# Performance work log

Measured on AMD Instinct MI355X. Metric: run time of the kernel, lower is better.

Reference implementation:

```python
import jax, jax.numpy as jnp
import numpy as np

BLOCK = 32      # block_size
KB = 128        # K // BLOCK (mask rows)
NB = 128        # N // BLOCK (mask cols)
DENSITY = 0.1


def _make_mask_indices():
    rng = np.random.RandomState(0)
    mask = rng.rand(KB, NB) < DENSITY
    # guarantee no fully-empty output column (kernel writes zeros there anyway,
    # segment_sum also yields zeros, so this is only to keep stats sane)
    ii, jj = np.nonzero(mask)   # row-major order == torch.nonzero(mask)
    return ii.astype(np.int32), jj.astype(np.int32)


def setup_inputs() -> dict:
    key = jax.random.key(0)
    k1, k2 = jax.random.split(key)
    ii, jj = _make_mask_indices()
    nnz = ii.shape[0]
    M = 4096
    K = KB * BLOCK
    x = jax.random.normal(k1, (M, K), dtype=jnp.float32)
    # block-sparse weight: one [BLOCK, BLOCK] tile per nonzero mask entry,
    # stored in row-major nonzero order (matches torch.nonzero ordering)
    w = jax.random.normal(k2, (nnz, BLOCK, BLOCK), dtype=jnp.float32) * 0.02
    return {"x": x, "w": w, "idx_i": jnp.asarray(ii), "idx_j": jnp.asarray(jj)}


def reference(x, w, idx_i, idx_j):
    # y[:, j*B:(j+1)*B] += x[:, i*B:(i+1)*B] @ w[blk] for each nonzero block (i, j)
    M, K = x.shape
    nnz, B, _ = w.shape
    xb = x.reshape(M, K // B, B)[:, idx_i, :]                 # [M, nnz, B] gather
    partial = jnp.einsum('mnk,nkj->nmj', xb, w)               # [nnz, M, B]
    yb = jax.ops.segment_sum(partial, idx_j, num_segments=NB)  # [NB, M, B] scatter-add
    return yb.transpose(1, 0, 2).reshape(M, NB * B)           # [M, N]
```

## Files before the change

kernel.cpp:

```cpp
#include <hip/hip_runtime.h>
#include <hip/hip_bf16.h>

typedef __bf16 bf16x8 __attribute__((ext_vector_type(8)));
typedef __bf16 bf16x4 __attribute__((ext_vector_type(4)));
typedef float f32x4 __attribute__((ext_vector_type(4)));

#define KDIM 4096
#define NDIM 4096
#define NBJ  128
#define KB   128

__global__ __launch_bounds__(256) void k_prep(
    const float* __restrict__ x, const float* __restrict__ w,
    const int* __restrict__ idx_i, const int* __restrict__ idx_j,
    __bf16* __restrict__ xb, __bf16* __restrict__ wT,
    int* __restrict__ colptr, int* __restrict__ colinfo,
    int nnz, int M, int nbCvt) {
    __shared__ char smem[2176];
    int b = blockIdx.x, t = threadIdx.x;

    if (b < nbCvt) {
        int i  = b & (KB - 1);
        int m0 = (b >> 7) * 64;
        int q  = t & 3, r = t >> 2;
        const float* xp = x + (size_t)(m0 + r) * KDIM + i * 32 + q * 8;
        float4 u = ((const float4*)xp)[0];
        float4 v = ((const float4*)xp)[1];
        bf16x8 o;
        o[0]=(__bf16)u.x; o[1]=(__bf16)u.y; o[2]=(__bf16)u.z; o[3]=(__bf16)u.w;
        o[4]=(__bf16)v.x; o[5]=(__bf16)v.y; o[6]=(__bf16)v.z; o[7]=(__bf16)v.w;
        *(bf16x8*)(xb + ((size_t)i * M + m0 + r) * 32 + q * 8) = o;
    } else if (b < nbCvt + nnz) {
        auto tile = (__bf16(*)[33])smem;
        int n = b - nbCvt;
        float4 v = ((const float4*)(w + (size_t)n * 1024))[t];
        int e = t * 4, k = e >> 5, c = e & 31;
        tile[k][c + 0] = (__bf16)v.x; tile[k][c + 1] = (__bf16)v.y;
        tile[k][c + 2] = (__bf16)v.z; tile[k][c + 3] = (__bf16)v.w;
        __syncthreads();
        int f = t * 4, cc = f >> 5, kk = f & 31;
        bf16x4 o;
        o[0] = tile[kk + 0][cc]; o[1] = tile[kk + 1][cc];
        o[2] = tile[kk + 2][cc]; o[3] = tile[kk + 3][cc];
        ((bf16x4*)(wT + (size_t)n * 1024))[t] = o;
    } else {
        int* cnt = (int*)smem;
        int* cur = cnt + NBJ;
        if (t < NBJ) cnt[t] = 0;
        __syncthreads();
        for (int n = t; n < nnz; n += 256) atomicAdd(&cnt[idx_j[n]], 1);
        __syncthreads();
        int mycount = (t < NBJ) ? cnt[t] : 0;
        for (int off = 1; off < NBJ; off <<= 1) {
            int add = (t < NBJ && t >= off) ? cnt[t - off] : 0;
            __syncthreads();
            if (t < NBJ) cnt[t] += add;
            __syncthreads();
        }
        if (t < NBJ) {
            colptr[t + 1] = cnt[t];
            cur[t] = cnt[t] - mycount;
            if (t == 0) colptr[0] = 0;
        }
        __syncthreads();
        for (int n = t; n < nnz; n += 256) {
            int j = idx_j[n];
            int pos = atomicAdd(&cur[j], 1);
            colinfo[pos] = (idx_i[n] << 16) | n;
        }
    }
}

struct Frag { bf16x8 a0, a1, a2, a3, b0, b1; };

__global__ __launch_bounds__(256) void k_bsmm(
    const __bf16* __restrict__ xb, const __bf16* __restrict__ wT,
    const int* __restrict__ colptr, const int* __restrict__ colinfo,
    float* __restrict__ y, int M) {
    int RCH = M >> 8;
    int l = blockIdx.x;
    int rc, j;
    if ((RCH & 7) == 0) {
        int rps = RCH >> 3;
        int s = l & 7, u = l >> 3;
        rc = s * rps + (u % rps);
        j  = u / rps;
    } else {
        rc = l % RCH; j = l / RCH;
    }
    int lane = threadIdx.x & 63, wave = threadIdx.x >> 6;
    int quad = lane >> 4, l16 = lane & 15;
    int wrow = rc * 256 + wave * 64;

    int beg = colptr[j], end = colptr[j + 1];
    int cnt = end - beg;

    f32x4 acc[4][2] = {};

    if (cnt > 0) {
        size_t strideA = (size_t)M * 32;
        const __bf16* xbase = xb + (size_t)(wrow + l16) * 32 + quad * 8;
        const __bf16* wbase = wT + l16 * 32 + quad * 8;
        int cap = cnt - 1;

        if (cnt <= 64) {
            int einfo = colinfo[beg + (lane <= cap ? lane : cap)];
            auto fetch = [&](int p) {
                int pp = p <= cap ? p : cap;
                int ee = __shfl(einfo, pp);
                int n = ee & 0xFFFF, ib = ee >> 16;
                Frag f;
                const __bf16* xp = xbase + (size_t)ib * strideA;
                f.a0 = *(const bf16x8*)(xp);
                f.a1 = *(const bf16x8*)(xp + 16 * 32);
                f.a2 = *(const bf16x8*)(xp + 32 * 32);
                f.a3 = *(const bf16x8*)(xp + 48 * 32);
                const __bf16* wp = wbase + (size_t)n * 1024;
                f.b0 = *(const bf16x8*)(wp);
                f.b1 = *(const bf16x8*)(wp + 512);
                return f;
            };
            Frag f0 = fetch(0);
            Frag f1 = fetch(1);
            for (int p = 0; p < cnt; ++p) {
                acc[0][0] = __builtin_amdgcn_mfma_f32_16x16x32_bf16(f0.a0, f0.b0, acc[0][0], 0, 0, 0);
                acc[0][1] = __builtin_amdgcn_mfma_f32_16x16x32_bf16(f0.a0, f0.b1, acc[0][1], 0, 0, 0);
                acc[1][0] = __builtin_amdgcn_mfma_f32_16x16x32_bf16(f0.a1, f0.b0, acc[1][0], 0, 0, 0);
                acc[1][1] = __builtin_amdgcn_mfma_f32_16x16x32_bf16(f0.a1, f0.b1, acc[1][1], 0, 0, 0);
                acc[2][0] = __builtin_amdgcn_mfma_f32_16x16x32_bf16(f0.a2, f0.b0, acc[2][0], 0, 0, 0);
                acc[2][1] = __builtin_amdgcn_mfma_f32_16x16x32_bf16(f0.a2, f0.b1, acc[2][1], 0, 0, 0);
                acc[3][0] = __builtin_amdgcn_mfma_f32_16x16x32_bf16(f0.a3, f0.b0, acc[3][0], 0, 0, 0);
                acc[3][1] = __builtin_amdgcn_mfma_f32_16x16x32_bf16(f0.a3, f0.b1, acc[3][1], 0, 0, 0);
                f0 = f1;
                f1 = fetch(p + 2);
            }
        } else {
            auto fetch = [&](int p) {
                int pp = p <= cap ? p : cap;
                int ee = colinfo[beg + pp];
                int n = ee & 0xFFFF, ib = ee >> 16;
                Frag f;
                const __bf16* xp = xbase + (size_t)ib * strideA;
                f.a0 = *(const bf16x8*)(xp);
                f.a1 = *(const bf16x8*)(xp + 16 * 32);
                f.a2 = *(const bf16x8*)(xp + 32 * 32);
                f.a3 = *(const bf16x8*)(xp + 48 * 32);
                const __bf16* wp = wbase + (size_t)n * 1024;
                f.b0 = *(const bf16x8*)(wp);
                f.b1 = *(const bf16x8*)(wp + 512);
                return f;
            };
            Frag f0 = fetch(0);
            Frag f1 = fetch(1);
            for (int p = 0; p < cnt; ++p) {
                acc[0][0] = __builtin_amdgcn_mfma_f32_16x16x32_bf16(f0.a0, f0.b0, acc[0][0], 0, 0, 0);
                acc[0][1] = __builtin_amdgcn_mfma_f32_16x16x32_bf16(f0.a0, f0.b1, acc[0][1], 0, 0, 0);
                acc[1][0] = __builtin_amdgcn_mfma_f32_16x16x32_bf16(f0.a1, f0.b0, acc[1][0], 0, 0, 0);
                acc[1][1] = __builtin_amdgcn_mfma_f32_16x16x32_bf16(f0.a1, f0.b1, acc[1][1], 0, 0, 0);
                acc[2][0] = __builtin_amdgcn_mfma_f32_16x16x32_bf16(f0.a2, f0.b0, acc[2][0], 0, 0, 0);
                acc[2][1] = __builtin_amdgcn_mfma_f32_16x16x32_bf16(f0.a2, f0.b1, acc[2][1], 0, 0, 0);
                acc[3][0] = __builtin_amdgcn_mfma_f32_16x16x32_bf16(f0.a3, f0.b0, acc[3][0], 0, 0, 0);
                acc[3][1] = __builtin_amdgcn_mfma_f32_16x16x32_bf16(f0.a3, f0.b1, acc[3][1], 0, 0, 0);
                f0 = f1;
                f1 = fetch(p + 2);
            }
        }
    }

    #pragma unroll
    for (int r = 0; r < 4; ++r)
        #pragma unroll
        for (int ch = 0; ch < 2; ++ch)
            #pragma unroll
            for (int reg = 0; reg < 4; ++reg) {
                int row = wrow + r * 16 + quad * 4 + reg;
                int col = j * 32 + ch * 16 + l16;
                y[(size_t)row * NDIM + col] = acc[r][ch][reg];
            }
}

__global__ __launch_bounds__(256) void k_bsmm_nows(
    const float* __restrict__ x, const float* __restrict__ w,
    const int* __restrict__ idx_i, const int* __restrict__ idx_j,
    float* __restrict__ y, int nnz) {
    __shared__ int list[256];
    __shared__ int listn;
    __shared__ __bf16 tw[32][40];
    int j = blockIdx.y;
    int tid = threadIdx.x;
    int lane = tid & 63, wave = tid >> 6;
    int quad = lane >> 4, l16 = lane & 15;
    int wrow = blockIdx.x * 256 + wave * 64;

    if (tid == 0) listn = 0;
    __syncthreads();
    for (int n = tid; n < nnz; n += 256)
        if (idx_j[n] == j) { int p = atomicAdd(&listn, 1); list[p & 255] = n; }
    __syncthreads();
    int cnt = listn;

    f32x4 acc[4][2] = {};
    for (int p = 0; p < cnt; ++p) {
        int n = list[p];
        int ib = idx_i[n];
        {
            float4 v = ((const float4*)(w + (size_t)n * 1024))[tid];
            int e = tid * 4, k = e >> 5, c = e & 31;
            tw[c + 0][k] = (__bf16)v.x; tw[c + 1][k] = (__bf16)v.y;
            tw[c + 2][k] = (__bf16)v.z; tw[c + 3][k] = (__bf16)v.w;
        }
        __syncthreads();
        bf16x8 a[4];
        #pragma unroll
        for (int r = 0; r < 4; ++r) {
            const float* xp = x + (size_t)(wrow + r * 16 + l16) * KDIM + ib * 32 + quad * 8;
            float4 u = *(const float4*)(xp);
            float4 v = *(const float4*)(xp + 4);
            a[r][0] = (__bf16)u.x; a[r][1] = (__bf16)u.y; a[r][2] = (__bf16)u.z; a[r][3] = (__bf16)u.w;
            a[r][4] = (__bf16)v.x; a[r][5] = (__bf16)v.y; a[r][6] = (__bf16)v.z; a[r][7] = (__bf16)v.w;
        }
        bf16x8 b0 = *(const bf16x8*)&tw[l16][quad * 8];
        bf16x8 b1 = *(const bf16x8*)&tw[l16 + 16][quad * 8];
        #pragma unroll
        for (int r = 0; r < 4; ++r) {
            acc[r][0] = __builtin_amdgcn_mfma_f32_16x16x32_bf16(a[r], b0, acc[r][0], 0, 0, 0);
            acc[r][1] = __builtin_amdgcn_mfma_f32_16x16x32_bf16(a[r], b1, acc[r][1], 0, 0, 0);
        }
        __syncthreads();
    }

    #pragma unroll
    for (int r = 0; r < 4; ++r)
        #pragma unroll
        for (int ch = 0; ch < 2; ++ch)
            #pragma unroll
            for (int reg = 0; reg < 4; ++reg) {
                int row = wrow + r * 16 + quad * 4 + reg;
                int col = j * 32 + ch * 16 + l16;
                y[(size_t)row * NDIM + col] = acc[r][ch][reg];
            }
}

extern "C" void kernel_launch(void* const* d_in, const int* in_sizes, int n_in,
                              void* d_out, int out_size, void* d_ws, size_t ws_size,
                              hipStream_t stream) {
    const float* x     = (const float*)d_in[0];
    const float* w     = (const float*)d_in[1];
    const int*   idx_i = (const int*)d_in[2];
    const int*   idx_j = (const int*)d_in[3];
    float*       y     = (float*)d_out;

    int nnz = in_sizes[2];
    int M   = in_sizes[0] / KDIM;

    size_t xb_bytes = (size_t)M * KDIM * 2;
    size_t wt_bytes = (size_t)nnz * 1024 * 2;
    size_t need = xb_bytes + wt_bytes + (size_t)(NBJ + 2 + nnz) * 4;

    if (ws_size >= need && (M & 255) == 0) {
        __bf16* xb      = (__bf16*)d_ws;
        __bf16* wT      = (__bf16*)((char*)d_ws + xb_bytes);
        int*    colptr  = (int*)((char*)d_ws + xb_bytes + wt_bytes);
        int*    colinfo = colptr + NBJ + 1;
        int nbCvt = KB * (M / 64);
        k_prep<<<nbCvt + nnz + 1, 256, 0, stream>>>(x, w, idx_i, idx_j,
                                                    xb, wT, colptr, colinfo,
                                                    nnz, M, nbCvt);
        k_bsmm<<<(M / 256) * NBJ, 256, 0, stream>>>(xb, wT, colptr, colinfo, y, M);
    } else {
        k_bsmm_nows<<<dim3(M / 256, NBJ), 256, 0, stream>>>(x, w, idx_i, idx_j, y, nnz);
    }
}
```

Baseline: 172.4 us.

## Fuse prep and block-sparse matmul into one cooperative kernel with grid sync

Replaces the separate conversion/CSR-build kernel and the MFMA matmul kernel with a single cooperative kernel. Each block first converts its slice of x to bf16, some blocks transpose weight tiles, and the last block builds column pointers, then a grid-wide sync precedes the matmul tile. This removes a kernel launch boundary and the tail/launch gap between them, at the cost of a grid barrier and requiring all 2048 blocks to be co-resident (launch bounds raised to 8 blocks per CU), which may increase register pressure. Falls back to the two-kernel path if the cooperative launch fails.

```diff
diff --git a/kernel.cpp b/kernel.cpp
--- a/kernel.cpp
+++ b/kernel.cpp
@@ -1,5 +1,8 @@
 #include <hip/hip_runtime.h>
+#include <hip/hip_cooperative_groups.h>
 #include <hip/hip_bf16.h>
+
+namespace cg = cooperative_groups;
 
 typedef __bf16 bf16x8 __attribute__((ext_vector_type(8)));
 typedef __bf16 bf16x4 __attribute__((ext_vector_type(4)));
@@ -9,6 +12,183 @@
 #define NDIM 4096
 #define NBJ  128
 #define KB   128
+
+__device__ __forceinline__ void bsmm_tile(
+    const __bf16* __restrict__ xb, const __bf16* __restrict__ wT,
+    const int* __restrict__ colptr, const int* __restrict__ colinfo,
+    float* __restrict__ y, int M, int rc, int j) {
+    int lane = threadIdx.x & 63, wave = threadIdx.x >> 6;
+    int quad = lane >> 4, l16 = lane & 15;
+    int wrow = rc * 256 + wave * 64;
+
+    int beg = colptr[j], end = colptr[j + 1];
+    int cnt = end - beg;
+
+    f32x4 acc[4][2] = {};
+
+    if (cnt > 0) {
+        size_t strideA = (size_t)M * 32;
+        const __bf16* xbase = xb + (size_t)(wrow + l16) * 32 + quad * 8;
+        const __bf16* wbase = wT + l16 * 32 + quad * 8;
+        int cap = cnt - 1;
+
+        if (cnt <= 64) {
+            int einfo = colinfo[beg + (lane <= cap ? lane : cap)];
+            auto fetch = [&](int p) {
+                int pp = p <= cap ? p : cap;
+                int ee = __shfl(einfo, pp);
+                int n = ee & 0xFFFF, ib = ee >> 16;
+                struct { bf16x8 a0, a1, a2, a3, b0, b1; } f;
+                const __bf16* xp = xbase + (size_t)ib * strideA;
+                f.a0 = *(const bf16x8*)(xp);
+                f.a1 = *(const bf16x8*)(xp + 16 * 32);
+                f.a2 = *(const bf16x8*)(xp + 32 * 32);
+                f.a3 = *(const bf16x8*)(xp + 48 * 32);
+                const __bf16* wp = wbase + (size_t)n * 1024;
+                f.b0 = *(const bf16x8*)(wp);
+                f.b1 = *(const bf16x8*)(wp + 512);
+                return f;
+            };
+            auto f0 = fetch(0);
+            auto f1 = fetch(1);
+            for (int p = 0; p < cnt; ++p) {
+                acc[0][0] = __builtin_amdgcn_mfma_f32_16x16x32_bf16(f0.a0, f0.b0, acc[0][0], 0, 0, 0);
+                acc[0][1] = __builtin_amdgcn_mfma_f32_16x16x32_bf16(f0.a0, f0.b1, acc[0][1], 0, 0, 0);
+                acc[1][0] = __builtin_amdgcn_mfma_f32_16x16x32_bf16(f0.a1, f0.b0, acc[1][0], 0, 0, 0);
+                acc[1][1] = __builtin_amdgcn_mfma_f32_16x16x32_bf16(f0.a1, f0.b1, acc[1][1], 0, 0, 0);
+                acc[2][0] = __builtin_amdgcn_mfma_f32_16x16x32_bf16(f0.a2, f0.b0, acc[2][0], 0, 0, 0);
+                acc[2][1] = __builtin_amdgcn_mfma_f32_16x16x32_bf16(f0.a2, f0.b1, acc[2][1], 0, 0, 0);
+                acc[3][0] = __builtin_amdgcn_mfma_f32_16x16x32_bf16(f0.a3, f0.b0, acc[3][0], 0, 0, 0);
+                acc[3][1] = __builtin_amdgcn_mfma_f32_16x16x32_bf16(f0.a3, f0.b1, acc[3][1], 0, 0, 0);
+                f0 = f1;
+                f1 = fetch(p + 2);
+            }
+        } else {
+            auto fetch = [&](int p) {
+                int pp = p <= cap ? p : cap;
+                int ee = colinfo[beg + pp];
+                int n = ee & 0xFFFF, ib = ee >> 16;
+                struct { bf16x8 a0, a1, a2, a3, b0, b1; } f;
+                const __bf16* xp = xbase + (size_t)ib * strideA;
+                f.a0 = *(const bf16x8*)(xp);
+                f.a1 = *(const bf16x8*)(xp + 16 * 32);
+                f.a2 = *(const bf16x8*)(xp + 32 * 32);
+                f.a3 = *(const bf16x8*)(xp + 48 * 32);
+                const __bf16* wp = wbase + (size_t)n * 1024;
+                f.b0 = *(const bf16x8*)(wp);
+                f.b1 = *(const bf16x8*)(wp + 512);
+                return f;
+            };
+            auto f0 = fetch(0);
+            auto f1 = fetch(1);
+            for (int p = 0; p < cnt; ++p) {
+                acc[0][0] = __builtin_amdgcn_mfma_f32_16x16x32_bf16(f0.a0, f0.b0, acc[0][0], 0, 0, 0);
+                acc[0][1] = __builtin_amdgcn_mfma_f32_16x16x32_bf16(f0.a0, f0.b1, acc[0][1], 0, 0, 0);
+                acc[1][0] = __builtin_amdgcn_mfma_f32_16x16x32_bf16(f0.a1, f0.b0, acc[1][0], 0, 0, 0);
+                acc[1][1] = __builtin_amdgcn_mfma_f32_16x16x32_bf16(f0.a1, f0.b1, acc[1][1], 0, 0, 0);
+                acc[2][0] = __builtin_amdgcn_mfma_f32_16x16x32_bf16(f0.a2, f0.b0, acc[2][0], 0, 0, 0);
+                acc[2][1] = __builtin_amdgcn_mfma_f32_16x16x32_bf16(f0.a2, f0.b1, acc[2][1], 0, 0, 0);
+                acc[3][0] = __builtin_amdgcn_mfma_f32_16x16x32_bf16(f0.a3, f0.b0, acc[3][0], 0, 0, 0);
+                acc[3][1] = __builtin_amdgcn_mfma_f32_16x16x32_bf16(f0.a3, f0.b1, acc[3][1], 0, 0, 0);
+                f0 = f1;
+                f1 = fetch(p + 2);
+            }
+        }
+    }
+
+    #pragma unroll
+    for (int r = 0; r < 4; ++r)
+        #pragma unroll
+        for (int ch = 0; ch < 2; ++ch)
+            #pragma unroll
+            for (int reg = 0; reg < 4; ++reg) {
+                int row = wrow + r * 16 + quad * 4 + reg;
+                int col = j * 32 + ch * 16 + l16;
+                y[(size_t)row * NDIM + col] = acc[r][ch][reg];
+            }
+}
+
+__global__ __launch_bounds__(256, 8) void k_fused(
+    const float* __restrict__ x, const float* __restrict__ w,
+    const int* __restrict__ idx_i, const int* __restrict__ idx_j,
+    __bf16* __restrict__ xb, __bf16* __restrict__ wT,
+    int* __restrict__ colptr, int* __restrict__ colinfo,
+    float* __restrict__ y, int nnz, int M) {
+    __shared__ char smem[2176];
+    int l = blockIdx.x, t = threadIdx.x;
+    int RCH = M >> 8;
+
+    int rc, j;
+    if ((RCH & 7) == 0) {
+        int rps = RCH >> 3;
+        int s = l & 7, u = l >> 3;
+        rc = s * rps + (u % rps);
+        j  = u / rps;
+    } else {
+        rc = l % RCH; j = l / RCH;
+    }
+
+    {
+        int q = t & 3, r = t >> 2;
+        #pragma unroll
+        for (int it = 0; it < 4; ++it) {
+            int row = rc * 256 + it * 64 + r;
+            const float* xp = x + (size_t)row * KDIM + j * 32 + q * 8;
+            float4 u4 = ((const float4*)xp)[0];
+            float4 v4 = ((const float4*)xp)[1];
+            bf16x8 o;
+            o[0]=(__bf16)u4.x; o[1]=(__bf16)u4.y; o[2]=(__bf16)u4.z; o[3]=(__bf16)u4.w;
+            o[4]=(__bf16)v4.x; o[5]=(__bf16)v4.y; o[6]=(__bf16)v4.z; o[7]=(__bf16)v4.w;
+            *(bf16x8*)(xb + ((size_t)j * M + row) * 32 + q * 8) = o;
+        }
+    }
+
+    for (int n = l; n < nnz; n += gridDim.x) {
+        auto tile = (__bf16(*)[33])smem;
+        float4 v = ((const float4*)(w + (size_t)n * 1024))[t];
+        int e = t * 4, k = e >> 5, c = e & 31;
+        tile[k][c + 0] = (__bf16)v.x; tile[k][c + 1] = (__bf16)v.y;
+        tile[k][c + 2] = (__bf16)v.z; tile[k][c + 3] = (__bf16)v.w;
+        __syncthreads();
+        int f = t * 4, cc = f >> 5, kk = f & 31;
+        bf16x4 o;
+        o[0] = tile[kk + 0][cc]; o[1] = tile[kk + 1][cc];
+        o[2] = tile[kk + 2][cc]; o[3] = tile[kk + 3][cc];
+        ((bf16x4*)(wT + (size_t)n * 1024))[t] = o;
+        __syncthreads();
+    }
+
+    if (l == gridDim.x - 1) {
+        int* cnt = (int*)smem;
+        int* cur = cnt + NBJ;
+        if (t < NBJ) cnt[t] = 0;
+        __syncthreads();
+        for (int n = t; n < nnz; n += 256) atomicAdd(&cnt[idx_j[n]], 1);
+        __syncthreads();
+        int mycount = (t < NBJ) ? cnt[t] : 0;
+        for (int off = 1; off < NBJ; off <<= 1) {
+            int add = (t < NBJ && t >= off) ? cnt[t - off] : 0;
+            __syncthreads();
+            if (t < NBJ) cnt[t] += add;
+            __syncthreads();
+        }
+        if (t < NBJ) {
+            colptr[t + 1] = cnt[t];
+            cur[t] = cnt[t] - mycount;
+            if (t == 0) colptr[0] = 0;
+        }
+        __syncthreads();
+        for (int n = t; n < nnz; n += 256) {
+            int jj = idx_j[n];
+            int pos = atomicAdd(&cur[jj], 1);
+            colinfo[pos] = (idx_i[n] << 16) | n;
+        }
+    }
+
+    cg::this_grid().sync();
+
+    bsmm_tile(xb, wT, colptr, colinfo, y, M, rc, j);
+}
 
 __global__ __launch_bounds__(256) void k_prep(
     const float* __restrict__ x, const float* __restrict__ w,
@@ -64,14 +244,12 @@
         }
         __syncthreads();
         for (int n = t; n < nnz; n += 256) {
-            int j = idx_j[n];
-            int pos = atomicAdd(&cur[j], 1);
+            int jj = idx_j[n];
+            int pos = atomicAdd(&cur[jj], 1);
             colinfo[pos] = (idx_i[n] << 16) | n;
         }
     }
 }
-
-struct Frag { bf16x8 a0, a1, a2, a3, b0, b1; };
 
 __global__ __launch_bounds__(256) void k_bsmm(
     const __bf16* __restrict__ xb, const __bf16* __restrict__ wT,
@@ -88,95 +266,7 @@
     } else {
         rc = l % RCH; j = l / RCH;
     }
-    int lane = threadIdx.x & 63, wave = threadIdx.x >> 6;
-    int quad = lane >> 4, l16 = lane & 15;
-    int wrow = rc * 256 + wave * 64;
-
-    int beg = colptr[j], end = colptr[j + 1];
-    int cnt = end - beg;
-
-    f32x4 acc[4][2] = {};
-
-    if (cnt > 0) {
-        size_t strideA = (size_t)M * 32;
-        const __bf16* xbase = xb + (size_t)(wrow + l16) * 32 + quad * 8;
-        const __bf16* wbase = wT + l16 * 32 + quad * 8;
-        int cap = cnt - 1;
-
-        if (cnt <= 64) {
-            int einfo = colinfo[beg + (lane <= cap ? lane : cap)];
-            auto fetch = [&](int p) {
-                int pp = p <= cap ? p : cap;
-                int ee = __shfl(einfo, pp);
-                int n = ee & 0xFFFF, ib = ee >> 16;
-                Frag f;
-                const __bf16* xp = xbase + (size_t)ib * strideA;
-                f.a0 = *(const bf16x8*)(xp);
-                f.a1 = *(const bf16x8*)(xp + 16 * 32);
-                f.a2 = *(const bf16x8*)(xp + 32 * 32);
-                f.a3 = *(const bf16x8*)(xp + 48 * 32);
-                const __bf16* wp = wbase + (size_t)n * 1024;
-                f.b0 = *(const bf16x8*)(wp);
-                f.b1 = *(const bf16x8*)(wp + 512);
-                return f;
-            };
-            Frag f0 = fetch(0);
-            Frag f1 = fetch(1);
-            for (int p = 0; p < cnt; ++p) {
-                acc[0][0] = __builtin_amdgcn_mfma_f32_16x16x32_bf16(f0.a0, f0.b0, acc[0][0], 0, 0, 0);
-                acc[0][1] = __builtin_amdgcn_mfma_f32_16x16x32_bf16(f0.a0, f0.b1, acc[0][1], 0, 0, 0);
-                acc[1][0] = __builtin_amdgcn_mfma_f32_16x16x32_bf16(f0.a1, f0.b0, acc[1][0], 0, 0, 0);
-                acc[1][1] = __builtin_amdgcn_mfma_f32_16x16x32_bf16(f0.a1, f0.b1, acc[1][1], 0, 0, 0);
-                acc[2][0] = __builtin_amdgcn_mfma_f32_16x16x32_bf16(f0.a2, f0.b0, acc[2][0], 0, 0, 0);
-                acc[2][1] = __builtin_amdgcn_mfma_f32_16x16x32_bf16(f0.a2, f0.b1, acc[2][1], 0, 0, 0);
-                acc[3][0] = __builtin_amdgcn_mfma_f32_16x16x32_bf16(f0.a3, f0.b0, acc[3][0], 0, 0, 0);
-                acc[3][1] = __builtin_amdgcn_mfma_f32_16x16x32_bf16(f0.a3, f0.b1, acc[3][1], 0, 0, 0);
-                f0 = f1;
-                f1 = fetch(p + 2);
-            }
-        } else {
-            auto fetch = [&](int p) {
-                int pp = p <= cap ? p : cap;
-                int ee = colinfo[beg + pp];
-                int n = ee & 0xFFFF, ib = ee >> 16;
-                Frag f;
-                const __bf16* xp = xbase + (size_t)ib * strideA;
-                f.a0 = *(const bf16x8*)(xp);
-                f.a1 = *(const bf16x8*)(xp + 16 * 32);
-                f.a2 = *(const bf16x8*)(xp + 32 * 32);
-                f.a3 = *(const bf16x8*)(xp + 48 * 32);
-                const __bf16* wp = wbase + (size_t)n * 1024;
-                f.b0 = *(const bf16x8*)(wp);
-                f.b1 = *(const bf16x8*)(wp + 512);
-                return f;
-            };
-            Frag f0 = fetch(0);
-            Frag f1 = fetch(1);
-            for (int p = 0; p < cnt; ++p) {
-                acc[0][0] = __builtin_amdgcn_mfma_f32_16x16x32_bf16(f0.a0, f0.b0, acc[0][0], 0, 0, 0);
-                acc[0][1] = __builtin_amdgcn_mfma_f32_16x16x32_bf16(f0.a0, f0.b1, acc[0][1], 0, 0, 0);
-                acc[1][0] = __builtin_amdgcn_mfma_f32_16x16x32_bf16(f0.a1, f0.b0, acc[1][0], 0, 0, 0);
-                acc[1][1] = __builtin_amdgcn_mfma_f32_16x16x32_bf16(f0.a1, f0.b1, acc[1][1], 0, 0, 0);
-                acc[2][0] = __builtin_amdgcn_mfma_f32_16x16x32_bf16(f0.a2, f0.b0, acc[2][0], 0, 0, 0);
-                acc[2][1] = __builtin_amdgcn_mfma_f32_16x16x32_bf16(f0.a2, f0.b1, acc[2][1], 0, 0, 0);
-                acc[3][0] = __builtin_amdgcn_mfma_f32_16x16x32_bf16(f0.a3, f0.b0, acc[3][0], 0, 0, 0);
-                acc[3][1] = __builtin_amdgcn_mfma_f32_16x16x32_bf16(f0.a3, f0.b1, acc[3][1], 0, 0, 0);
-                f0 = f1;
-                f1 = fetch(p + 2);
-            }
-        }
-    }
-
-    #pragma unroll
-    for (int r = 0; r < 4; ++r)
-        #pragma unroll
-        for (int ch = 0; ch < 2; ++ch)
-            #pragma unroll
-            for (int reg = 0; reg < 4; ++reg) {
-                int row = wrow + r * 16 + quad * 4 + reg;
-                int col = j * 32 + ch * 16 + l16;
-                y[(size_t)row * NDIM + col] = acc[r][ch][reg];
-            }
+    bsmm_tile(xb, wT, colptr, colinfo, y, M, rc, j);
 }
 
 __global__ __launch_bounds__(256) void k_bsmm_nows(
@@ -262,11 +352,21 @@
         __bf16* wT      = (__bf16*)((char*)d_ws + xb_bytes);
         int*    colptr  = (int*)((char*)d_ws + xb_bytes + wt_bytes);
         int*    colinfo = colptr + NBJ + 1;
-        int nbCvt = KB * (M / 64);
-        k_prep<<<nbCvt + nnz + 1, 256, 0, stream>>>(x, w, idx_i, idx_j,
-                                                    xb, wT, colptr, colinfo,
-                                                    nnz, M, nbCvt);
-        k_bsmm<<<(M / 256) * NBJ, 256, 0, stream>>>(xb, wT, colptr, colinfo, y, M);
+
+        int grid = (M / 256) * NBJ;
+        void* args[] = {(void*)&x, (void*)&w, (void*)&idx_i, (void*)&idx_j,
+                        (void*)&xb, (void*)&wT, (void*)&colptr, (void*)&colinfo,
+                        (void*)&y, (void*)&nnz, (void*)&M};
+        hipError_t err = hipLaunchCooperativeKernel(
+            (const void*)k_fused, dim3(grid), dim3(256), args, 0, stream);
+        if (err != hipSuccess) {
+            (void)hipGetLastError();
+            int nbCvt = KB * (M / 64);
+            k_prep<<<nbCvt + nnz + 1, 256, 0, stream>>>(x, w, idx_i, idx_j,
+                                                        xb, wT, colptr, colinfo,
+                                                        nnz, M, nbCvt);
+            k_bsmm<<<(M / 256) * NBJ, 256, 0, stream>>>(xb, wT, colptr, colinfo, y, M);
+        }
     } else {
         k_bsmm_nows<<<dim3(M / 256, NBJ), 256, 0, stream>>>(x, w, idx_i, idx_j, y, nnz);
     }
```

Result: slower. 429.9 us (+149.4%).

## Stage weight blocks in padded LDS per column and deepen A-fragment prefetch

Applied to the files above, without the earlier changes.

The bsmm kernel now loads batches of up to 14 weight tiles for its output column into shared memory, padded to avoid bank conflicts, and has all four waves read B fragments from LDS. Previously each wave fetched them from global memory. The A-fragment prefetch grows from two to three stages, the block-index mapping becomes j-major using shifts and masks, and launch bounds request 4 blocks per CU. This should cut redundant global weight traffic and hide x-load latency better, at the cost of extra barriers per batch and about 35 KB of LDS per block, which may limit occupancy.

```diff
diff --git a/kernel.cpp b/kernel.cpp
--- a/kernel.cpp
+++ b/kernel.cpp
@@ -9,6 +9,9 @@
 #define NDIM 4096
 #define NBJ  128
 #define KB   128
+
+#define NB      14
+#define BLK_LDS 2560
 
 __global__ __launch_bounds__(256) void k_prep(
     const float* __restrict__ x, const float* __restrict__ w,
@@ -71,99 +74,83 @@
     }
 }
 
-struct Frag { bf16x8 a0, a1, a2, a3, b0, b1; };
-
-__global__ __launch_bounds__(256) void k_bsmm(
+struct AFrag { bf16x8 a0, a1, a2, a3; };
+
+#define MFMA8(A, B0, B1)                                                       \
+    acc[0][0] = __builtin_amdgcn_mfma_f32_16x16x32_bf16(A.a0, B0, acc[0][0], 0, 0, 0); \
+    acc[0][1] = __builtin_amdgcn_mfma_f32_16x16x32_bf16(A.a0, B1, acc[0][1], 0, 0, 0); \
+    acc[1][0] = __builtin_amdgcn_mfma_f32_16x16x32_bf16(A.a1, B0, acc[1][0], 0, 0, 0); \
+    acc[1][1] = __builtin_amdgcn_mfma_f32_16x16x32_bf16(A.a1, B1, acc[1][1], 0, 0, 0); \
+    acc[2][0] = __builtin_amdgcn_mfma_f32_16x16x32_bf16(A.a2, B0, acc[2][0], 0, 0, 0); \
+    acc[2][1] = __builtin_amdgcn_mfma_f32_16x16x32_bf16(A.a2, B1, acc[2][1], 0, 0, 0); \
+    acc[3][0] = __builtin_amdgcn_mfma_f32_16x16x32_bf16(A.a3, B0, acc[3][0], 0, 0, 0); \
+    acc[3][1] = __builtin_amdgcn_mfma_f32_16x16x32_bf16(A.a3, B1, acc[3][1], 0, 0, 0);
+
+__global__ __launch_bounds__(256, 4) void k_bsmm(
     const __bf16* __restrict__ xb, const __bf16* __restrict__ wT,
     const int* __restrict__ colptr, const int* __restrict__ colinfo,
     float* __restrict__ y, int M) {
+    __shared__ int nfo[NB];
+    __shared__ __attribute__((aligned(16))) char wbuf[NB * BLK_LDS];
+
     int RCH = M >> 8;
     int l = blockIdx.x;
     int rc, j;
     if ((RCH & 7) == 0) {
         int rps = RCH >> 3;
         int s = l & 7, u = l >> 3;
-        rc = s * rps + (u % rps);
-        j  = u / rps;
+        rc = s * rps + (u >> 7);
+        j  = u & (NBJ - 1);
     } else {
         rc = l % RCH; j = l / RCH;
     }
-    int lane = threadIdx.x & 63, wave = threadIdx.x >> 6;
+    int t = threadIdx.x;
+    int lane = t & 63, wave = t >> 6;
     int quad = lane >> 4, l16 = lane & 15;
     int wrow = rc * 256 + wave * 64;
 
     int beg = colptr[j], end = colptr[j + 1];
-    int cnt = end - beg;
 
     f32x4 acc[4][2] = {};
 
-    if (cnt > 0) {
-        size_t strideA = (size_t)M * 32;
-        const __bf16* xbase = xb + (size_t)(wrow + l16) * 32 + quad * 8;
-        const __bf16* wbase = wT + l16 * 32 + quad * 8;
-        int cap = cnt - 1;
-
-        if (cnt <= 64) {
-            int einfo = colinfo[beg + (lane <= cap ? lane : cap)];
-            auto fetch = [&](int p) {
-                int pp = p <= cap ? p : cap;
-                int ee = __shfl(einfo, pp);
-                int n = ee & 0xFFFF, ib = ee >> 16;
-                Frag f;
-                const __bf16* xp = xbase + (size_t)ib * strideA;
-                f.a0 = *(const bf16x8*)(xp);
-                f.a1 = *(const bf16x8*)(xp + 16 * 32);
-                f.a2 = *(const bf16x8*)(xp + 32 * 32);
-                f.a3 = *(const bf16x8*)(xp + 48 * 32);
-                const __bf16* wp = wbase + (size_t)n * 1024;
-                f.b0 = *(const bf16x8*)(wp);
-                f.b1 = *(const bf16x8*)(wp + 512);
-                return f;
-            };
-            Frag f0 = fetch(0);
-            Frag f1 = fetch(1);
-            for (int p = 0; p < cnt; ++p) {
-                acc[0][0] = __builtin_amdgcn_mfma_f32_16x16x32_bf16(f0.a0, f0.b0, acc[0][0], 0, 0, 0);
-                acc[0][1] = __builtin_amdgcn_mfma_f32_16x16x32_bf16(f0.a0, f0.b1, acc[0][1], 0, 0, 0);
-                acc[1][0] = __builtin_amdgcn_mfma_f32_16x16x32_bf16(f0.a1, f0.b0, acc[1][0], 0, 0, 0);
-                acc[1][1] = __builtin_amdgcn_mfma_f32_16x16x32_bf16(f0.a1, f0.b1, acc[1][1], 0, 0, 0);
-                acc[2][0] = __builtin_amdgcn_mfma_f32_16x16x32_bf16(f0.a2, f0.b0, acc[2][0], 0, 0, 0);
-                acc[2][1] = __builtin_amdgcn_mfma_f32_16x16x32_bf16(f0.a2, f0.b1, acc[2][1], 0, 0, 0);
-                acc[3][0] = __builtin_amdgcn_mfma_f32_16x16x32_bf16(f0.a3, f0.b0, acc[3][0], 0, 0, 0);
-                acc[3][1] = __builtin_amdgcn_mfma_f32_16x16x32_bf16(f0.a3, f0.b1, acc[3][1], 0, 0, 0);
-                f0 = f1;
-                f1 = fetch(p + 2);
-            }
-        } else {
-            auto fetch = [&](int p) {
-                int pp = p <= cap ? p : cap;
-                int ee = colinfo[beg + pp];
-                int n = ee & 0xFFFF, ib = ee >> 16;
-                Frag f;
-                const __bf16* xp = xbase + (size_t)ib * strideA;
-                f.a0 = *(const bf16x8*)(xp);
-                f.a1 = *(const bf16x8*)(xp + 16 * 32);
-                f.a2 = *(const bf16x8*)(xp + 32 * 32);
-                f.a3 = *(const bf16x8*)(xp + 48 * 32);
-                const __bf16* wp = wbase + (size_t)n * 1024;
-                f.b0 = *(const bf16x8*)(wp);
-                f.b1 = *(const bf16x8*)(wp + 512);
-                return f;
-            };
-            Frag f0 = fetch(0);
-            Frag f1 = fetch(1);
-            for (int p = 0; p < cnt; ++p) {
-                acc[0][0] = __builtin_amdgcn_mfma_f32_16x16x32_bf16(f0.a0, f0.b0, acc[0][0], 0, 0, 0);
-                acc[0][1] = __builtin_amdgcn_mfma_f32_16x16x32_bf16(f0.a0, f0.b1, acc[0][1], 0, 0, 0);
-                acc[1][0] = __builtin_amdgcn_mfma_f32_16x16x32_bf16(f0.a1, f0.b0, acc[1][0], 0, 0, 0);
-                acc[1][1] = __builtin_amdgcn_mfma_f32_16x16x32_bf16(f0.a1, f0.b1, acc[1][1], 0, 0, 0);
-                acc[2][0] = __builtin_amdgcn_mfma_f32_16x16x32_bf16(f0.a2, f0.b0, acc[2][0], 0, 0, 0);
-                acc[2][1] = __builtin_amdgcn_mfma_f32_16x16x32_bf16(f0.a2, f0.b1, acc[2][1], 0, 0, 0);
-                acc[3][0] = __builtin_amdgcn_mfma_f32_16x16x32_bf16(f0.a3, f0.b0, acc[3][0], 0, 0, 0);
-                acc[3][1] = __builtin_amdgcn_mfma_f32_16x16x32_bf16(f0.a3, f0.b1, acc[3][1], 0, 0, 0);
-                f0 = f1;
-                f1 = fetch(p + 2);
-            }
+    size_t strideA = (size_t)M * 32;
+    const __bf16* xbase = xb + (size_t)(wrow + l16) * 32 + quad * 8;
+    const char*   wread = wbuf + l16 * 80 + quad * 16;
+
+    for (int bb = beg; bb < end; bb += NB) {
+        int cb = end - bb; if (cb > NB) cb = NB;
+        if (bb > beg) __syncthreads();
+        if (t < cb) nfo[t] = colinfo[bb + t];
+        __syncthreads();
+
+        for (int c = t; c < cb * 128; c += 256) {
+            int b = c >> 7, w16 = c & 127;
+            int n = nfo[b] & 0xFFFF;
+            bf16x8 v = *(const bf16x8*)(wT + (size_t)n * 1024 + w16 * 8);
+            *(bf16x8*)(wbuf + b * BLK_LDS + (w16 >> 2) * 80 + (w16 & 3) * 16) = v;
+        }
+        __syncthreads();
+
+        auto fa = [&](int p) {
+            int pp = p < cb ? p : cb - 1;
+            int ib = nfo[pp] >> 16;
+            AFrag f;
+            const __bf16* xp = xbase + (size_t)ib * strideA;
+            f.a0 = *(const bf16x8*)(xp);
+            f.a1 = *(const bf16x8*)(xp + 16 * 32);
+            f.a2 = *(const bf16x8*)(xp + 32 * 32);
+            f.a3 = *(const bf16x8*)(xp + 48 * 32);
+            return f;
+        };
+        AFrag A0 = fa(0);
+        AFrag A1 = fa(1);
+        AFrag A2 = fa(2);
+        for (int p = 0; p < cb; ++p) {
+            const char* wp = wread + p * BLK_LDS;
+            bf16x8 b0 = *(const bf16x8*)(wp);
+            bf16x8 b1 = *(const bf16x8*)(wp + 16 * 80);
+            MFMA8(A0, b0, b1);
+            A0 = A1; A1 = A2; A2 = fa(p + 3);
         }
     }
 
@@ -257,7 +244,7 @@
     size_t wt_bytes = (size_t)nnz * 1024 * 2;
     size_t need = xb_bytes + wt_bytes + (size_t)(NBJ + 2 + nnz) * 4;
 
-    if (ws_size >= need && (M & 255) == 0) {
+    if (ws_size >= need && (M & 255) == 0 && nnz < 65536) {
         __bf16* xb      = (__bf16*)d_ws;
         __bf16* wT      = (__bf16*)((char*)d_ws + xb_bytes);
         int*    colptr  = (int*)((char*)d_ws + xb_bytes + wt_bytes);
```

Result: faster. 166.8 us (-3.2%).
